# Performance work log

Hardware: AMD Instinct MI355X
Metric: run time of the kernel (lower is better)

The kernel has to match this reference:

```python
import jax, jax.numpy as jnp
import numpy as np

N_POOL = 500_000   # number of source neurons (value store size)
N_W = 1024         # number of unique (deduplicated) weight matrices
E = 1_000_000      # number of connections (neuron-input pairs)
D_IN = 16
D_OUT = 16


def setup_inputs() -> dict:
    key = jax.random.key(0)
    k1, k2, k3, k4 = jax.random.split(key, 4)
    values = jax.random.normal(k1, (N_POOL, D_IN), dtype=jnp.float32)
    weight = jax.random.normal(k2, (N_W, D_OUT, D_IN), dtype=jnp.float32)
    input_idx = jax.random.randint(k3, (E,), 0, N_POOL, dtype=jnp.int64) if jax.config.jax_enable_x64 else jax.random.randint(k3, (E,), 0, N_POOL).astype(jnp.int32)
    weight_idx = jax.random.randint(k4, (E,), 0, N_W).astype(jnp.int32)
    return {"values": values, "weight": weight, "input_idx": input_idx, "weight_idx": weight_idx}


def reference(values, weight, input_idx, weight_idx):
    # LINEAR_GATHER: gather input value vectors per connection  -> [E, D_IN]
    x = values[input_idx]
    # LINEAR_WEIGHTS_GATHER: gather weight matrices per connection -> [E, D_OUT, D_IN]
    w = weight[weight_idx]
    # LINEAR_LINEAR: per-connection matmul (w @ input_values) -> [E, D_OUT]
    y = jnp.einsum('eoi,ei->eo', w, x)
    return y
```

## Files before the change

kernel.cpp:

```cpp
#include <hip/hip_runtime.h>


#define D 16
#define BPB 4

__device__ __forceinline__ float4 wload(const float* __restrict__ weight,
                                        int wi, int lane) {
    return ((const float4*)(weight + (long long)wi * (D * D)))[lane];
}

#define WLOAD8(C0, W0,W1,W2,W3,W4,W5,W6,W7) do {                               \
    W0 = wload(weight, __builtin_amdgcn_readlane(wcur, (C0)+0), lane);         \
    W1 = wload(weight, __builtin_amdgcn_readlane(wcur, (C0)+1), lane);         \
    W2 = wload(weight, __builtin_amdgcn_readlane(wcur, (C0)+2), lane);         \
    W3 = wload(weight, __builtin_amdgcn_readlane(wcur, (C0)+3), lane);         \
    W4 = wload(weight, __builtin_amdgcn_readlane(wcur, (C0)+4), lane);         \
    W5 = wload(weight, __builtin_amdgcn_readlane(wcur, (C0)+5), lane);         \
    W6 = wload(weight, __builtin_amdgcn_readlane(wcur, (C0)+6), lane);         \
    W7 = wload(weight, __builtin_amdgcn_readlane(wcur, (C0)+7), lane);         \
} while (0)

#define CONN1(C, WV) do {                                                      \
    const float4 xv = *(const float4*)(&xbuf[(C) * D + ((q ^ ((C) >> 4)) << 2)]); \
    float p = WV.x*xv.x + WV.y*xv.y + WV.z*xv.z + WV.w*xv.w;                   \
    p += __shfl_xor(p, 1);                                                     \
    p += __shfl_xor(p, 2);                                                     \
    if (q == 0 && (C) < nb) out[(long long)(k0 + (C)) * D + r] = p;            \
} while (0)

#define CONN8(C0, W0,W1,W2,W3,W4,W5,W6,W7) do {                                \
    CONN1((C0)+0, W0); CONN1((C0)+1, W1); CONN1((C0)+2, W2); CONN1((C0)+3, W3);\
    CONN1((C0)+4, W4); CONN1((C0)+5, W5); CONN1((C0)+6, W6); CONN1((C0)+7, W7);\
} while (0)

__global__ __launch_bounds__(64, 4) void direct_mv(
    const float* __restrict__ values, const float* __restrict__ weight,
    const int* __restrict__ iidx, const int* __restrict__ widx,
    float* __restrict__ out, int E)
{
    __shared__ float xbuf[64 * D];
    const int lane = threadIdx.x;
    const int g4 = lane >> 2;
    const int q  = lane & 3;
    const int r  = g4;

    int s0 = blockIdx.x * (64 * BPB);
    if (s0 >= E) return;
    int s1 = min(E, s0 + 64 * BPB);

    int iv, wnext;
    float4 xq0, xq1, xq2, xq3;
    {
        int kl = s0 + lane; if (kl >= s1) kl = s1 - 1;
        iv    = iidx[kl];
        wnext = widx[kl];
        int iiu;
        iiu = __shfl(iv,      g4); xq0 = ((const float4*)(values + (long long)iiu * D))[q];
        iiu = __shfl(iv, 16 + g4); xq1 = ((const float4*)(values + (long long)iiu * D))[q];
        iiu = __shfl(iv, 32 + g4); xq2 = ((const float4*)(values + (long long)iiu * D))[q];
        iiu = __shfl(iv, 48 + g4); xq3 = ((const float4*)(values + (long long)iiu * D))[q];
    }

    for (int k0 = s0; k0 < s1; k0 += 64) {
        ((float4*)&xbuf[( 0 + g4) * D])[q ^ 0] = xq0;
        ((float4*)&xbuf[(16 + g4) * D])[q ^ 1] = xq1;
        ((float4*)&xbuf[(32 + g4) * D])[q ^ 2] = xq2;
        ((float4*)&xbuf[(48 + g4) * D])[q ^ 3] = xq3;
        int wcur = wnext;
        int nb = s1 - k0; if (nb > 64) nb = 64;

        int kn = k0 + 64;
        if (kn < s1) {
            int kl = kn + lane; if (kl >= s1) kl = s1 - 1;
            iv    = iidx[kl];
            wnext = widx[kl];
            int iiu;
            iiu = __shfl(iv,      g4); xq0 = ((const float4*)(values + (long long)iiu * D))[q];
            iiu = __shfl(iv, 16 + g4); xq1 = ((const float4*)(values + (long long)iiu * D))[q];
            iiu = __shfl(iv, 32 + g4); xq2 = ((const float4*)(values + (long long)iiu * D))[q];
            iiu = __shfl(iv, 48 + g4); xq3 = ((const float4*)(values + (long long)iiu * D))[q];
        }

        float4 A0,A1,A2,A3,A4,A5,A6,A7;
        float4 B0,B1,B2,B3,B4,B5,B6,B7;
        WLOAD8( 0, A0,A1,A2,A3,A4,A5,A6,A7);
        WLOAD8( 8, B0,B1,B2,B3,B4,B5,B6,B7);
        CONN8 ( 0, A0,A1,A2,A3,A4,A5,A6,A7);
        WLOAD8(16, A0,A1,A2,A3,A4,A5,A6,A7);
        CONN8 ( 8, B0,B1,B2,B3,B4,B5,B6,B7);
        WLOAD8(24, B0,B1,B2,B3,B4,B5,B6,B7);
        CONN8 (16, A0,A1,A2,A3,A4,A5,A6,A7);
        WLOAD8(32, A0,A1,A2,A3,A4,A5,A6,A7);
        CONN8 (24, B0,B1,B2,B3,B4,B5,B6,B7);
        WLOAD8(40, B0,B1,B2,B3,B4,B5,B6,B7);
        CONN8 (32, A0,A1,A2,A3,A4,A5,A6,A7);
        WLOAD8(48, A0,A1,A2,A3,A4,A5,A6,A7);
        CONN8 (40, B0,B1,B2,B3,B4,B5,B6,B7);
        WLOAD8(56, B0,B1,B2,B3,B4,B5,B6,B7);
        CONN8 (48, A0,A1,A2,A3,A4,A5,A6,A7);
        CONN8 (56, B0,B1,B2,B3,B4,B5,B6,B7);
    }
}

extern "C" void kernel_launch(void* const* d_in, const int* in_sizes, int n_in,
                              void* d_out, int out_size, void* d_ws, size_t ws_size,
                              hipStream_t stream) {
    const float* values     = (const float*)d_in[0];
    const float* weight     = (const float*)d_in[1];
    const int*   input_idx  = (const int*)d_in[2];
    const int*   weight_idx = (const int*)d_in[3];
    float*       out        = (float*)d_out;

    int E = in_sizes[2];
    if (E <= 0) return;
    int nblk = (E + 64 * BPB - 1) / (64 * BPB);
    hipLaunchKernelGGL(direct_mv, dim3(nblk), dim3(64), 0, stream,
                       values, weight, input_idx, weight_idx, out, E);
}
```

Baseline: 150.7 us.

## Switch to persistent grid-stride multi-wave blocks for connection batches

Replaces the single-wave blocks that each handled four contiguous 64-connection batches with 256-thread blocks of four independent waves. The grid is capped at 2048 blocks and each wave walks batches in grid-stride order, prefetching the next batch's gather while computing the current one. This cuts the number of block launches and gives each wave a longer software pipeline, at the cost of less locality between consecutive batches and a possible tail imbalance.

```diff
diff --git a/kernel.cpp b/kernel.cpp
--- a/kernel.cpp
+++ b/kernel.cpp
@@ -2,7 +2,9 @@
 
 
 #define D 16
-#define BPB 4
+#define WPB 4
+#define TPB (WPB * 64)
+#define MAXBLK 2048
 
 __device__ __forceinline__ float4 wload(const float* __restrict__ weight,
                                         int wi, int lane) {
@@ -33,53 +35,50 @@
     CONN1((C0)+4, W4); CONN1((C0)+5, W5); CONN1((C0)+6, W6); CONN1((C0)+7, W7);\
 } while (0)
 
-__global__ __launch_bounds__(64, 4) void direct_mv(
+#define GATHER(BI) do {                                                        \
+    int kl = (BI) * 64 + lane; if (kl >= E) kl = E - 1;                        \
+    iv    = iidx[kl];                                                          \
+    wnext = widx[kl];                                                          \
+    int iiu;                                                                   \
+    iiu = __shfl(iv,      g4); xq0 = ((const float4*)(values + (long long)iiu * D))[q]; \
+    iiu = __shfl(iv, 16 + g4); xq1 = ((const float4*)(values + (long long)iiu * D))[q]; \
+    iiu = __shfl(iv, 32 + g4); xq2 = ((const float4*)(values + (long long)iiu * D))[q]; \
+    iiu = __shfl(iv, 48 + g4); xq3 = ((const float4*)(values + (long long)iiu * D))[q]; \
+} while (0)
+
+__global__ __launch_bounds__(TPB, 8) void direct_mv(
     const float* __restrict__ values, const float* __restrict__ weight,
     const int* __restrict__ iidx, const int* __restrict__ widx,
     float* __restrict__ out, int E)
 {
-    __shared__ float xbuf[64 * D];
-    const int lane = threadIdx.x;
+    __shared__ float xbuf_all[WPB * 64 * D];
+    const int lane = threadIdx.x & 63;
+    const int wid  = threadIdx.x >> 6;
+    float* xbuf = xbuf_all + wid * (64 * D);
     const int g4 = lane >> 2;
     const int q  = lane & 3;
     const int r  = g4;
 
-    int s0 = blockIdx.x * (64 * BPB);
-    if (s0 >= E) return;
-    int s1 = min(E, s0 + 64 * BPB);
+    const int nbatch = (E + 63) >> 6;
+    const int gw = blockIdx.x * WPB + wid;
+    const int GW = gridDim.x * WPB;
+    if (gw >= nbatch) return;
 
     int iv, wnext;
     float4 xq0, xq1, xq2, xq3;
-    {
-        int kl = s0 + lane; if (kl >= s1) kl = s1 - 1;
-        iv    = iidx[kl];
-        wnext = widx[kl];
-        int iiu;
-        iiu = __shfl(iv,      g4); xq0 = ((const float4*)(values + (long long)iiu * D))[q];
-        iiu = __shfl(iv, 16 + g4); xq1 = ((const float4*)(values + (long long)iiu * D))[q];
-        iiu = __shfl(iv, 32 + g4); xq2 = ((const float4*)(values + (long long)iiu * D))[q];
-        iiu = __shfl(iv, 48 + g4); xq3 = ((const float4*)(values + (long long)iiu * D))[q];
-    }
+    GATHER(gw);
 
-    for (int k0 = s0; k0 < s1; k0 += 64) {
+    for (int bi = gw; bi < nbatch; bi += GW) {
         ((float4*)&xbuf[( 0 + g4) * D])[q ^ 0] = xq0;
         ((float4*)&xbuf[(16 + g4) * D])[q ^ 1] = xq1;
         ((float4*)&xbuf[(32 + g4) * D])[q ^ 2] = xq2;
         ((float4*)&xbuf[(48 + g4) * D])[q ^ 3] = xq3;
         int wcur = wnext;
-        int nb = s1 - k0; if (nb > 64) nb = 64;
+        int k0 = bi * 64;
+        int nb = E - k0; if (nb > 64) nb = 64;
 
-        int kn = k0 + 64;
-        if (kn < s1) {
-            int kl = kn + lane; if (kl >= s1) kl = s1 - 1;
-            iv    = iidx[kl];
-            wnext = widx[kl];
-            int iiu;
-            iiu = __shfl(iv,      g4); xq0 = ((const float4*)(values + (long long)iiu * D))[q];
-            iiu = __shfl(iv, 16 + g4); xq1 = ((const float4*)(values + (long long)iiu * D))[q];
-            iiu = __shfl(iv, 32 + g4); xq2 = ((const float4*)(values + (long long)iiu * D))[q];
-            iiu = __shfl(iv, 48 + g4); xq3 = ((const float4*)(values + (long long)iiu * D))[q];
-        }
+        int bn = bi + GW;
+        if (bn < nbatch) GATHER(bn);
 
         float4 A0,A1,A2,A3,A4,A5,A6,A7;
         float4 B0,B1,B2,B3,B4,B5,B6,B7;
@@ -113,7 +112,9 @@
 
     int E = in_sizes[2];
     if (E <= 0) return;
-    int nblk = (E + 64 * BPB - 1) / (64 * BPB);
-    hipLaunchKernelGGL(direct_mv, dim3(nblk), dim3(64), 0, stream,
+    int nbatch = (E + 63) >> 6;
+    int nblk = (nbatch + WPB - 1) / WPB;
+    if (nblk > MAXBLK) nblk = MAXBLK;
+    hipLaunchKernelGGL(direct_mv, dim3(nblk), dim3(TPB), 0, stream,
                        values, weight, input_idx, weight_idx, out, E);
 }
```

Result: slower. 344.5 us (+128.7%).
